# Kernel optimization log

Measured on AMD Instinct MI355X. Metric: run time of the kernel, lower is better.

## Reference

```python
import jax, jax.numpy as jnp
import numpy as np

N, M, D = 8192, 8192, 512
TINY = jnp.finfo(jnp.float32).tiny


def setup_inputs() -> dict:
    key = jax.random.key(0)
    k1, k2 = jax.random.split(key)
    x = jax.random.normal(k1, (N, D), dtype=jnp.float32)
    x2 = jax.random.normal(k2, (M, D), dtype=jnp.float32)
    # flax self.param with ones initializer (pre-softplus raw params)
    amplitude_raw = jnp.ones((1,), dtype=jnp.float32)
    length_scale_raw = jnp.ones((D,), dtype=jnp.float32)
    return {"x": x, "x2": x2, "amplitude_raw": amplitude_raw,
            "length_scale_raw": length_scale_raw}


def reference(x, x2, amplitude_raw, length_scale_raw):
    # Parameter transforms exactly as in RBFKernelProvider.apply
    amplitude = jax.nn.softplus(amplitude_raw) + TINY          # (1,)
    length_scale = jax.nn.softplus(length_scale_raw) + TINY    # (D,)

    # rbf_kernel_fun: exp(-0.5 * sum(((x - x2)/l)^2)) * amp^2
    # GEMM rewrite of the squared scaled distance (avoids (N,M,D) intermediate):
    # ||xs_i - ys_j||^2 = ||xs_i||^2 + ||ys_j||^2 - 2 xs_i . ys_j
    xs = x / length_scale                                       # (N, D)
    ys = x2 / length_scale                                      # (M, D)
    x_sq = jnp.sum(xs * xs, axis=-1)                            # (N,)
    y_sq = jnp.sum(ys * ys, axis=-1)                            # (M,)
    cross = jnp.einsum('nd,md->nm', xs, ys)                     # (N, M) GEMM
    sq_dists = jnp.maximum(x_sq[:, None] + y_sq[None, :] - 2.0 * cross, 0.0)
    kernel_matrix = jnp.exp(-0.5 * sq_dists)                    # (N, M)
    return (amplitude ** 2) * kernel_matrix
```

## Files before the change

kernel.cpp:

```cpp
#include <hip/hip_runtime.h>

#define AS1 __attribute__((address_space(1)))
#define AS3 __attribute__((address_space(3)))

typedef __attribute__((ext_vector_type(4))) float f32x4;
typedef __attribute__((ext_vector_type(8))) int   i32x8;

static constexpr int Nn = 8192;
static constexpr int Mm = 8192;
static constexpr int Dd = 512;
static constexpr float TINY = 1.17549435082228751e-38f;

__device__ __forceinline__ float softplus_f(float x) {
    return fmaxf(x, 0.0f) + log1pf(expf(-fabsf(x)));
}

__device__ __forceinline__ void g2l16(const void* g, void* l) {
    __builtin_amdgcn_global_load_lds((const AS1 unsigned int*)g,
                                     (AS3 unsigned int*)l, 16, 0, 0);
}

__global__ __launch_bounds__(256) void scale_rows(
        const float* __restrict__ x, const float* __restrict__ x2,
        const float* __restrict__ ls_raw,
        unsigned char* __restrict__ xs, unsigned char* __restrict__ ys,
        float* __restrict__ x_sq, float* __restrict__ y_sq) {
    int wave = threadIdx.x >> 6, lane = threadIdx.x & 63;
    int row = blockIdx.x * 4 + wave;

    const float* src; unsigned char* dst; float* nrm; int r;
    if (row < Nn) {
        src = x  + (size_t)row * Dd; dst = xs + (size_t)row * 512;
        nrm = x_sq + row; r = row;
    } else {
        int m = row - Nn;
        src = x2 + (size_t)m * Dd;   dst = ys + (size_t)m * 512;
        nrm = y_sq + m; r = m;
    }

    float4 v0 = ((const float4*)src)[lane * 2];
    float4 v1 = ((const float4*)src)[lane * 2 + 1];
    float4 L0 = ((const float4*)ls_raw)[lane * 2];
    float4 L1 = ((const float4*)ls_raw)[lane * 2 + 1];

    float il[8] = {
        1.0f / (softplus_f(L0.x) + TINY), 1.0f / (softplus_f(L0.y) + TINY),
        1.0f / (softplus_f(L0.z) + TINY), 1.0f / (softplus_f(L0.w) + TINY),
        1.0f / (softplus_f(L1.x) + TINY), 1.0f / (softplus_f(L1.y) + TINY),
        1.0f / (softplus_f(L1.z) + TINY), 1.0f / (softplus_f(L1.w) + TINY) };
    float s[8] = { v0.x*il[0], v0.y*il[1], v0.z*il[2], v0.w*il[3],
                   v1.x*il[4], v1.y*il[5], v1.z*il[6], v1.w*il[7] };
    float sum = 0.0f;
#pragma unroll
    for (int i = 0; i < 8; ++i) sum += s[i] * s[i];

    int p0 = __builtin_amdgcn_cvt_pk_fp8_f32(s[0], s[1], 0, false);
    p0     = __builtin_amdgcn_cvt_pk_fp8_f32(s[2], s[3], p0, true);
    int p1 = __builtin_amdgcn_cvt_pk_fp8_f32(s[4], s[5], 0, false);
    p1     = __builtin_amdgcn_cvt_pk_fp8_f32(s[6], s[7], p1, true);

    int j    = lane >> 1;
    int phys = (j & ~7) | ((j & 7) ^ (r & 7));
    *(int2*)(dst + phys * 16 + (lane & 1) * 8) = make_int2(p0, p1);

#pragma unroll
    for (int off = 32; off > 0; off >>= 1) sum += __shfl_down(sum, off, 64);
    if (lane == 0) *nrm = sum;
}

__global__ __launch_bounds__(256) void gemm_rbf(
        const unsigned char* __restrict__ xs,
        const unsigned char* __restrict__ ys,
        const float* __restrict__ x_sq, const float* __restrict__ y_sq,
        const float* __restrict__ amp_raw, float* __restrict__ out) {

    __shared__ unsigned char sA[128 * 128];
    __shared__ unsigned char sB[128 * 128];

    const int tid  = threadIdx.x;
    const int wave = tid >> 6, lane = tid & 63;
    const int wy = wave >> 1, wx = wave & 1;
    const int lane15 = lane & 15, quad = lane >> 4;
    const int srow = lane >> 3, schunk = lane & 7;

    const size_t rowBase = (size_t)blockIdx.y * 128;
    const size_t colBase = (size_t)blockIdx.x * 128;

    f32x4 acc[4][4] = {};

    for (int kt = 0; kt < 4; ++kt) {
        __syncthreads();
        const size_t kOff = (size_t)kt * 128;
#pragma unroll
        for (int t = 0; t < 4; ++t) {
            int issue = wave * 4 + t;
            int rit = issue * 8 + srow;
            const unsigned char* ga =
                xs + (rowBase + rit) * 512 + kOff + schunk * 16;
            g2l16(ga, sA + issue * 1024);
            const unsigned char* gb =
                ys + (colBase + rit) * 512 + kOff + schunk * 16;
            g2l16(gb, sB + issue * 1024);
        }
        __syncthreads();

        i32x8 bF[4];
#pragma unroll
        for (int tx = 0; tx < 4; ++tx) {
            int rr = wx * 64 + tx * 16 + lane15;
            int x7 = rr & 7;
            int p0 = (quad * 2 + 0) ^ x7, p1 = (quad * 2 + 1) ^ x7;
            int4 lo = *(const int4*)(sB + rr * 128 + p0 * 16);
            int4 hi = *(const int4*)(sB + rr * 128 + p1 * 16);
            i32x8 f; f[0]=lo.x; f[1]=lo.y; f[2]=lo.z; f[3]=lo.w;
                     f[4]=hi.x; f[5]=hi.y; f[6]=hi.z; f[7]=hi.w;
            bF[tx] = f;
        }
#pragma unroll
        for (int ty = 0; ty < 4; ++ty) {
            int rr = wy * 64 + ty * 16 + lane15;
            int x7 = rr & 7;
            int p0 = (quad * 2 + 0) ^ x7, p1 = (quad * 2 + 1) ^ x7;
            int4 lo = *(const int4*)(sA + rr * 128 + p0 * 16);
            int4 hi = *(const int4*)(sA + rr * 128 + p1 * 16);
            i32x8 aF; aF[0]=lo.x; aF[1]=lo.y; aF[2]=lo.z; aF[3]=lo.w;
                      aF[4]=hi.x; aF[5]=hi.y; aF[6]=hi.z; aF[7]=hi.w;
#pragma unroll
            for (int tx = 0; tx < 4; ++tx)
                acc[ty][tx] = __builtin_amdgcn_mfma_scale_f32_16x16x128_f8f6f4(
                    aF, bF[tx], acc[ty][tx],
                    0 , 0 ,
                    0, 0x7F7F7F7F,
                    0, 0x7F7F7F7F);
        }
    }

    float a = softplus_f(amp_raw[0]) + TINY;
    const float amp2 = a * a;
#pragma unroll
    for (int ty = 0; ty < 4; ++ty) {
        const size_t r0 = rowBase + wy * 64 + ty * 16 + quad * 4;
        float xq[4];
#pragma unroll
        for (int i = 0; i < 4; ++i) xq[i] = x_sq[r0 + i];
#pragma unroll
        for (int tx = 0; tx < 4; ++tx) {
            const size_t gc = colBase + wx * 64 + tx * 16 + lane15;
            const float yq = y_sq[gc];
            float* o = out + r0 * (size_t)Mm + gc;
#pragma unroll
            for (int reg = 0; reg < 4; ++reg) {
                float sq = fmaxf(xq[reg] + yq - 2.0f * acc[ty][tx][reg], 0.0f);
                o[(size_t)reg * Mm] = amp2 * __expf(-0.5f * sq);
            }
        }
    }
}

__global__ __launch_bounds__(256) void rbf_fallback(
        const float* __restrict__ x, const float* __restrict__ x2,
        const float* __restrict__ amp_raw, const float* __restrict__ ls_raw,
        float* __restrict__ out) {
    __shared__ float il[Dd];
    __shared__ float sX[16 * Dd];
    __shared__ float sY[16 * Dd];
    int tid = threadIdx.x;
    for (int i = tid; i < Dd; i += 256)
        il[i] = 1.0f / (softplus_f(ls_raw[i]) + TINY);
    __syncthreads();
    int bR = blockIdx.y * 16, bC = blockIdx.x * 16;
    for (int i = tid; i < 16 * Dd; i += 256) {
        int r = i >> 9, c = i & (Dd - 1);
        sX[i] = x [(size_t)(bR + r) * Dd + c] * il[c];
        sY[i] = x2[(size_t)(bC + r) * Dd + c] * il[c];
    }
    __syncthreads();
    float a = softplus_f(amp_raw[0]) + TINY;
    float amp2 = a * a;
    int r = tid >> 4, c = tid & 15;
    float sq = 0.0f;
    for (int d = 0; d < Dd; ++d) {
        float df = sX[r * Dd + d] - sY[c * Dd + d];
        sq += df * df;
    }
    out[(size_t)(bR + r) * Mm + (bC + c)] = amp2 * __expf(-0.5f * sq);
}

extern "C" void kernel_launch(void* const* d_in, const int* in_sizes, int n_in,
                              void* d_out, int out_size, void* d_ws, size_t ws_size,
                              hipStream_t stream) {
    const float* x       = (const float*)d_in[0];
    const float* x2      = (const float*)d_in[1];
    const float* amp_raw = (const float*)d_in[2];
    const float* ls_raw  = (const float*)d_in[3];
    float* out = (float*)d_out;

    const size_t OFF_XSQ = 0;
    const size_t OFF_YSQ = OFF_XSQ + 8192 * 4;
    const size_t OFF_XS  = OFF_YSQ + 8192 * 4;
    const size_t OFF_YS  = OFF_XS + (size_t)Nn * Dd;
    const size_t NEED    = OFF_YS + (size_t)Mm * Dd;

    if (ws_size < NEED) {
        dim3 g(Mm / 16, Nn / 16);
        rbf_fallback<<<g, 256, 0, stream>>>(x, x2, amp_raw, ls_raw, out);
        return;
    }

    char* ws = (char*)d_ws;
    float* x_sq = (float*)(ws + OFF_XSQ);
    float* y_sq = (float*)(ws + OFF_YSQ);
    unsigned char* xs = (unsigned char*)(ws + OFF_XS);
    unsigned char* ys = (unsigned char*)(ws + OFF_YS);

    scale_rows<<<(Nn + Mm) / 4, 256, 0, stream>>>(x, x2, ls_raw, xs, ys, x_sq, y_sq);
    dim3 g(Mm / 128, Nn / 128);
    gemm_rbf<<<g, 256, 0, stream>>>(xs, ys, x_sq, y_sq, amp_raw, out);
}
```

Before: 330.4 us.

## Double-buffer LDS tiles, swizzle block order, hoist norms, use nontemporal stores

The GEMM+RBF kernel now keeps two LDS buffers, so the global-to-LDS load for the next K slice is issued before the MFMA work on the current slice, with one barrier per iteration. Workgroup indices are remapped so blocks that run close together share rows and columns, which should improve L2 reuse. The x_sq/y_sq norm loads and the amplitude softplus move ahead of the K loop, and output writes become nontemporal stores so the large output does not pollute the cache. The cost is double the LDS per block (64KB), which may cut occupancy, plus more registers for the hoisted norms.

```diff
diff --git a/kernel.cpp b/kernel.cpp
--- a/kernel.cpp
+++ b/kernel.cpp
@@ -74,8 +74,8 @@
         const float* __restrict__ x_sq, const float* __restrict__ y_sq,
         const float* __restrict__ amp_raw, float* __restrict__ out) {
 
-    __shared__ unsigned char sA[128 * 128];
-    __shared__ unsigned char sB[128 * 128];
+    __shared__ unsigned char sA[2][128 * 128];
+    __shared__ unsigned char sB[2][128 * 128];
 
     const int tid  = threadIdx.x;
     const int wave = tid >> 6, lane = tid & 63;
@@ -83,26 +83,46 @@
     const int lane15 = lane & 15, quad = lane >> 4;
     const int srow = lane >> 3, schunk = lane & 7;
 
-    const size_t rowBase = (size_t)blockIdx.y * 128;
-    const size_t colBase = (size_t)blockIdx.x * 128;
-
-    f32x4 acc[4][4] = {};
-
-    for (int kt = 0; kt < 4; ++kt) {
-        __syncthreads();
+    const unsigned lin = blockIdx.y * 64u + blockIdx.x;
+    const unsigned swz = (lin & 7u) * 512u + (lin >> 3);
+    const size_t rowBase = (size_t)(swz >> 6) * 128;
+    const size_t colBase = (size_t)(swz & 63u) * 128;
+
+    auto stage = [&](int buf, int kt) {
         const size_t kOff = (size_t)kt * 128;
 #pragma unroll
         for (int t = 0; t < 4; ++t) {
             int issue = wave * 4 + t;
             int rit = issue * 8 + srow;
-            const unsigned char* ga =
-                xs + (rowBase + rit) * 512 + kOff + schunk * 16;
-            g2l16(ga, sA + issue * 1024);
-            const unsigned char* gb =
-                ys + (colBase + rit) * 512 + kOff + schunk * 16;
-            g2l16(gb, sB + issue * 1024);
-        }
-        __syncthreads();
+            g2l16(xs + (rowBase + rit) * 512 + kOff + schunk * 16,
+                  sA[buf] + issue * 1024);
+            g2l16(ys + (colBase + rit) * 512 + kOff + schunk * 16,
+                  sB[buf] + issue * 1024);
+        }
+    };
+
+    float xq[4][4], yq[4];
+#pragma unroll
+    for (int ty = 0; ty < 4; ++ty) {
+        const size_t r0 = rowBase + wy * 64 + ty * 16 + quad * 4;
+#pragma unroll
+        for (int i = 0; i < 4; ++i) xq[ty][i] = x_sq[r0 + i];
+    }
+#pragma unroll
+    for (int tx = 0; tx < 4; ++tx)
+        yq[tx] = y_sq[colBase + wx * 64 + tx * 16 + lane15];
+    float a = softplus_f(amp_raw[0]) + TINY;
+    const float amp2 = a * a;
+
+    f32x4 acc[4][4] = {};
+
+    stage(0, 0);
+    __syncthreads();
+
+#pragma unroll
+    for (int kt = 0; kt < 4; ++kt) {
+        const int cur = kt & 1;
+        if (kt < 3) stage(cur ^ 1, kt + 1);
 
         i32x8 bF[4];
 #pragma unroll
@@ -110,8 +130,8 @@
             int rr = wx * 64 + tx * 16 + lane15;
             int x7 = rr & 7;
             int p0 = (quad * 2 + 0) ^ x7, p1 = (quad * 2 + 1) ^ x7;
-            int4 lo = *(const int4*)(sB + rr * 128 + p0 * 16);
-            int4 hi = *(const int4*)(sB + rr * 128 + p1 * 16);
+            int4 lo = *(const int4*)(sB[cur] + rr * 128 + p0 * 16);
+            int4 hi = *(const int4*)(sB[cur] + rr * 128 + p1 * 16);
             i32x8 f; f[0]=lo.x; f[1]=lo.y; f[2]=lo.z; f[3]=lo.w;
                      f[4]=hi.x; f[5]=hi.y; f[6]=hi.z; f[7]=hi.w;
             bF[tx] = f;
@@ -121,8 +141,8 @@
             int rr = wy * 64 + ty * 16 + lane15;
             int x7 = rr & 7;
             int p0 = (quad * 2 + 0) ^ x7, p1 = (quad * 2 + 1) ^ x7;
-            int4 lo = *(const int4*)(sA + rr * 128 + p0 * 16);
-            int4 hi = *(const int4*)(sA + rr * 128 + p1 * 16);
+            int4 lo = *(const int4*)(sA[cur] + rr * 128 + p0 * 16);
+            int4 hi = *(const int4*)(sA[cur] + rr * 128 + p1 * 16);
             i32x8 aF; aF[0]=lo.x; aF[1]=lo.y; aF[2]=lo.z; aF[3]=lo.w;
                       aF[4]=hi.x; aF[5]=hi.y; aF[6]=hi.z; aF[7]=hi.w;
 #pragma unroll
@@ -133,25 +153,22 @@
                     0, 0x7F7F7F7F,
                     0, 0x7F7F7F7F);
         }
-    }
-
-    float a = softplus_f(amp_raw[0]) + TINY;
-    const float amp2 = a * a;
+        __syncthreads();
+    }
+
 #pragma unroll
     for (int ty = 0; ty < 4; ++ty) {
         const size_t r0 = rowBase + wy * 64 + ty * 16 + quad * 4;
-        float xq[4];
-#pragma unroll
-        for (int i = 0; i < 4; ++i) xq[i] = x_sq[r0 + i];
 #pragma unroll
         for (int tx = 0; tx < 4; ++tx) {
             const size_t gc = colBase + wx * 64 + tx * 16 + lane15;
-            const float yq = y_sq[gc];
             float* o = out + r0 * (size_t)Mm + gc;
 #pragma unroll
             for (int reg = 0; reg < 4; ++reg) {
-                float sq = fmaxf(xq[reg] + yq - 2.0f * acc[ty][tx][reg], 0.0f);
-                o[(size_t)reg * Mm] = amp2 * __expf(-0.5f * sq);
+                float sq = fmaxf(xq[ty][reg] + yq[tx] - 2.0f * acc[ty][tx][reg],
+                                 0.0f);
+                __builtin_nontemporal_store(amp2 * __expf(-0.5f * sq),
+                                            o + (size_t)reg * Mm);
             }
         }
     }
```

New measurement: 343.7 us. 4.0% more time.
